# Optimization experiments

Measured on AMD Instinct MI355X. Metric: run time of the kernel, lower is better.

## Reference

```python
import jax, jax.numpy as jnp
import numpy as np


def setup_inputs() -> dict:
    key = jax.random.key(0)
    k1, k2, k3 = jax.random.split(key, 3)
    B, C, H, W = 64, 3, 512, 512
    n_segments, box, embed_dim = 1024, 16, 768
    img = jax.random.normal(k1, (B, C, H, W), dtype=jnp.float32)
    segments = jax.random.randint(k2, (B, H, W), 0, n_segments, dtype=jnp.int32)
    conv_w = jax.random.normal(k3, (embed_dim, C, box, box), dtype=jnp.float32) * 0.02
    return {"img": img, "segments": segments, "conv_w": conv_w, "n_segments": n_segments}


def reference(img, segments, conv_w, n_segments):
    # img: [B,C,H,W], segments: [B,H,W] int in [0,n_segments), conv_w: [E,C,box,box]
    B, C, H, W = img.shape
    E, _, box, _ = conv_w.shape
    half = box // 2

    # --- centroid per segment via scatter-add (equivalent to the one-hot mask-weighted sums) ---
    x_coords = jnp.broadcast_to(jnp.arange(W, dtype=jnp.float32)[None, :], (H, W)).reshape(-1)
    y_coords = jnp.broadcast_to(jnp.arange(H, dtype=jnp.float32)[:, None], (H, W)).reshape(-1)
    data = jnp.stack([x_coords, y_coords, jnp.ones_like(x_coords)], axis=-1)  # [H*W, 3]
    data = jnp.broadcast_to(data[None], (B, H * W, 3)).reshape(-1, 3)
    seg_ids = (segments.reshape(B, H * W) + jnp.arange(B, dtype=segments.dtype)[:, None] * n_segments).reshape(-1)
    sums = jax.ops.segment_sum(data, seg_ids, num_segments=B * n_segments)  # [B*S, 3]
    sums = sums.reshape(B, n_segments, 3)
    counts = jnp.clip(sums[..., 2], 1e-6, None)
    x_c = sums[..., 0] / counts  # [B, S]
    y_c = sums[..., 1] / counts

    # --- patch extraction at centroids from zero-padded image ---
    # x_min = floor((x_c + half) - half) = floor(x_c); x_c >= 0 so trunc == floor.
    x_min = jnp.floor(x_c).astype(jnp.int32)
    y_min = jnp.floor(y_c).astype(jnp.int32)
    img_padded = jnp.pad(img, ((0, 0), (0, 0), (half, half), (half, half)))

    def crop(im, y0, x0):  # im: [C, H+box, W+box]
        return jax.lax.dynamic_slice(im, (0, y0, x0), (C, box, box))

    crop_segs = jax.vmap(crop, in_axes=(None, 0, 0))          # over segments
    patches = jax.vmap(crop_segs)(img_padded, y_min, x_min)   # [B, S, C, box, box]

    # --- conv with kernel_size == box on box-sized patches == single dot per patch ---
    embeddings = jnp.einsum('bschw,echw->bse', patches, conv_w)  # [B, S, E]
    return embeddings
```

## Files before the change

kernel.cpp:

```cpp
#include <hip/hip_runtime.h>
#include <hip/hip_bf16.h>
#include <stdint.h>

#define B_   64
#define H_   512
#define W_   512
#define S_N  1024
#define E_N  768
#define K_N  768
#define HALF 8

typedef short bf16x8 __attribute__((ext_vector_type(8)));
typedef float f32x4  __attribute__((ext_vector_type(4)));
typedef float f32x4u __attribute__((ext_vector_type(4), aligned(4)));

__device__ __forceinline__ unsigned short f2bf(float f) {
  union { float f; unsigned u; } v; v.f = f;
  unsigned u = v.u;
  u += 0x7FFF + ((u >> 16) & 1);
  return (unsigned short)(u >> 16);
}

__global__ void k_accum_convw(const int* __restrict__ seg,
                              unsigned long long* __restrict__ partials,
                              const float* __restrict__ w,
                              unsigned short* __restrict__ wb) {
  __shared__ unsigned long long ls[S_N];
  const int bid = blockIdx.x;
  const int tid = threadIdx.x;
  if (bid >= 1024) {
    int idx = (bid - 1024) * 256 + tid;
    float4 v = ((const float4*)w)[idx];
    ushort4 o;
    o.x = f2bf(v.x); o.y = f2bf(v.y); o.z = f2bf(v.z); o.w = f2bf(v.w);
    ((ushort4*)wb)[idx] = o;
    return;
  }
  const int xblk = bid & 15;
  const int b    = bid >> 4;
  for (int i = tid; i < S_N; i += 256) ls[i] = 0ULL;
  __syncthreads();
  const int pix0 = xblk * 16384;
  const int4* segb = (const int4*)(seg + (size_t)b * (H_ * W_) + pix0);
  for (int it = 0; it < 16; ++it) {
    int4 s4 = segb[it * 256 + tid];
    int p0 = pix0 + (it * 256 + tid) * 4;
    unsigned long long base = ((unsigned long long)(unsigned)(p0 >> 9) << 39)
                            | ((unsigned long long)(unsigned)(p0 & (W_ - 1)) << 15)
                            | 1ULL;
    #pragma unroll
    for (int j = 0; j < 4; ++j) {
      int s = (&s4.x)[j];
      s = ((unsigned)s < S_N) ? s : 0;
      atomicAdd(&ls[s], base + ((unsigned long long)j << 15));
    }
  }
  __syncthreads();
  unsigned long long* gp = partials + ((size_t)b * 16 + xblk) * S_N;
  for (int s = tid; s < S_N; s += 256) gp[s] = ls[s];
}

__global__ __launch_bounds__(512) void k_gemmfg(
    const float* __restrict__ img,
    const unsigned long long* __restrict__ partials,
    const unsigned short* __restrict__ Bmat,
    float* __restrict__ out) {
  __shared__ unsigned short As[256 * 64];
  __shared__ unsigned short Bs[256 * 64];
  __shared__ int2 pc[256];
  const int tid  = threadIdx.x;
  const int wave = tid >> 6;
  const int lane = tid & 63;

  const int virt = (blockIdx.x & 7) * 96 + (blockIdx.x >> 3);
  const int bm = virt / 3;
  const int bn = virt - bm * 3;
  const int gm0 = bm * 256;
  const int gn0 = bn * 256;
  const int b   = bm >> 2;
  const float* ib = img + (size_t)b * 3 * H_ * W_;

  if (tid < 256) {
    const int s = (gm0 + tid) & (S_N - 1);
    unsigned c = 0, sx = 0, sy = 0;
    #pragma unroll
    for (int x = 0; x < 16; ++x) {
      unsigned long long v = partials[((size_t)b * 16 + x) * S_N + s];
      c  += (unsigned)(v & 0x7FFFULL);
      sx += (unsigned)((v >> 15) & 0xFFFFFFULL);
      sy += (unsigned)(v >> 39);
    }
    int xmin = 0, ymin = 0;
    if (c > 0) {
      float cf = (float)c;
      xmin = (int)floorf((float)sx / cf);
      ymin = (int)floorf((float)sy / cf);
    }
    pc[tid] = make_int2(xmin - HALF, ymin - HALF);
  }

  const int wr = wave >> 2;
  const int wc = wave & 3;
  const int rlo  = lane & 15;
  const int rsel = lane & 7;
  const int sub  = lane >> 4;
  int swz[2];
  swz[0] = ((0 + sub) ^ rsel) * 8;
  swz[1] = ((4 + sub) ^ rsel) * 8;

  f32x4 acc[8][4];
  #pragma unroll
  for (int i = 0; i < 8; ++i)
    #pragma unroll
    for (int j = 0; j < 4; ++j)
      acc[i][j] = (f32x4){0.f, 0.f, 0.f, 0.f};

  __syncthreads();

  for (int kt = 0; kt < 12; ++kt) {
    const int k0 = kt * 64;

    #pragma unroll
    for (int i = 0; i < 4; ++i) {
      int seg = i * 512 + tid;
      int row = seg >> 3;
      int csrc = (seg & 7) ^ (row & 7);
      const unsigned short* g = Bmat + (size_t)(gn0 + row) * K_N + k0 + csrc * 8;
      __builtin_amdgcn_global_load_lds((const __attribute__((address_space(1))) void*)g,
        (__attribute__((address_space(3))) void*)&Bs[(i * 512 + wave * 64) * 8], 16, 0, 0);
    }

    f32x4 ga[4][2];
    #pragma unroll
    for (int i = 0; i < 4; ++i) {
      int seg = i * 512 + tid;
      int row = seg >> 3;
      int cc  = seg & 7;
      int k = k0 + cc * 8;
      int ch = k >> 8, h = (k >> 4) & 15, w0 = k & 15;
      int2 p = pc[row];
      int y  = p.y + h;
      int x0 = p.x + w0;
      if (p.x >= 0 && p.x <= W_ - 16 && p.y >= 0 && p.y <= H_ - 16) {
        const float* rp = ib + (size_t)((ch << 9) + y) * W_ + x0;
        ga[i][0] = *(const f32x4u*)rp;
        ga[i][1] = *(const f32x4u*)(rp + 4);
      } else {
        bool yok = (unsigned)y < H_;
        const float* rp = ib + (size_t)((ch << 9) + (yok ? y : 0)) * W_;
        f32x4 lo, hi;
        #pragma unroll
        for (int j = 0; j < 4; ++j) {
          int x = x0 + j;
          lo[j] = (yok && (unsigned)x < W_) ? rp[x] : 0.f;
        }
        #pragma unroll
        for (int j = 0; j < 4; ++j) {
          int x = x0 + 4 + j;
          hi[j] = (yok && (unsigned)x < W_) ? rp[x] : 0.f;
        }
        ga[i][0] = lo;
        ga[i][1] = hi;
      }
    }
    #pragma unroll
    for (int i = 0; i < 4; ++i) {
      int seg = i * 512 + tid;
      int row = seg >> 3;
      int cc  = seg & 7;
      bf16x8 t;
      t[0] = (short)f2bf(ga[i][0][0]); t[1] = (short)f2bf(ga[i][0][1]);
      t[2] = (short)f2bf(ga[i][0][2]); t[3] = (short)f2bf(ga[i][0][3]);
      t[4] = (short)f2bf(ga[i][1][0]); t[5] = (short)f2bf(ga[i][1][1]);
      t[6] = (short)f2bf(ga[i][1][2]); t[7] = (short)f2bf(ga[i][1][3]);
      *(bf16x8*)&As[row * 64 + ((cc ^ (row & 7)) << 3)] = t;
    }

    asm volatile("s_waitcnt vmcnt(0) lgkmcnt(0)" ::: "memory");
    __syncthreads();

    #pragma unroll
    for (int kk = 0; kk < 2; ++kk) {
      bf16x8 av[8], bv[4];
      #pragma unroll
      for (int mi = 0; mi < 8; ++mi)
        av[mi] = *(const bf16x8*)&As[(wr * 128 + mi * 16 + rlo) * 64 + swz[kk]];
      #pragma unroll
      for (int ni = 0; ni < 4; ++ni)
        bv[ni] = *(const bf16x8*)&Bs[(wc * 64 + ni * 16 + rlo) * 64 + swz[kk]];
      __builtin_amdgcn_s_setprio(1);
      #pragma unroll
      for (int mi = 0; mi < 8; ++mi)
        #pragma unroll
        for (int ni = 0; ni < 4; ++ni)
          acc[mi][ni] = __builtin_amdgcn_mfma_f32_16x16x32_bf16(
              av[mi], bv[ni], acc[mi][ni], 0, 0, 0);
      __builtin_amdgcn_s_setprio(0);
    }

    __syncthreads();
  }

  const int row0 = gm0 + wr * 128 + (lane >> 4) * 4;
  const int col0 = gn0 + wc * 64 + (lane & 15);
  #pragma unroll
  for (int mi = 0; mi < 8; ++mi)
    #pragma unroll
    for (int ni = 0; ni < 4; ++ni)
      #pragma unroll
      for (int r = 0; r < 4; ++r)
        out[(size_t)(row0 + mi * 16 + r) * E_N + (col0 + ni * 16)] = acc[mi][ni][r];
}

extern "C" void kernel_launch(void* const* d_in, const int* in_sizes, int n_in,
                              void* d_out, int out_size, void* d_ws, size_t ws_size,
                              hipStream_t stream) {
  const float* img = (const float*)d_in[0];
  const int*   seg = (const int*)d_in[1];
  const float* cw  = (const float*)d_in[2];
  float* out = (float*)d_out;
  char* ws = (char*)d_ws;

  unsigned long long* partials = (unsigned long long*)ws;
  unsigned short* Bmat = (unsigned short*)(ws + 8388608);

  k_accum_convw<<<1600, 256, 0, stream>>>(seg, partials, cw, Bmat);
  k_gemmfg<<<768, 512, 0, stream>>>(img, partials, Bmat, out);
}
```

Before: 162.3 us.

## Prefetch next K-tile into registers while MFMA computes current tile

Restructures the GEMM main loop into a register-prefetch pipeline. The global loads for the next K-tile (image patch gather and B matrix) are issued before the MFMA work on the current tile, then converted and written to LDS after it. B loads switch from global_load_lds direct-to-LDS to register loads followed by LDS stores. Per-row pointers and in-bounds flags are hoisted out of the loop. The aim is to hide global memory latency behind compute, at the cost of more registers (which may limit occupancy at 512 threads) and an extra barrier per iteration.

```diff
diff --git a/kernel.cpp b/kernel.cpp
--- a/kernel.cpp
+++ b/kernel.cpp
@@ -60,7 +60,7 @@
   for (int s = tid; s < S_N; s += 256) gp[s] = ls[s];
 }
 
-__global__ __launch_bounds__(512) void k_gemmfg(
+__global__ __launch_bounds__(512) void k_gemmfg2(
     const float* __restrict__ img,
     const unsigned long long* __restrict__ partials,
     const unsigned short* __restrict__ Bmat,
@@ -117,67 +117,75 @@
 
   __syncthreads();
 
-  for (int kt = 0; kt < 12; ++kt) {
-    const int k0 = kt * 64;
-
+  const int cc0 = tid & 7;
+  const int rsub = tid >> 3;
+  int2 pi[4]; bool inti[4];
+  const float* arow[4];
+  const unsigned short* brow[4];
+  #pragma unroll
+  for (int i = 0; i < 4; ++i) {
+    int row = i * 64 + rsub;
+    int2 p = pc[row];
+    pi[i] = p;
+    inti[i] = (p.x >= 0 && p.x <= W_ - 16 && p.y >= 0 && p.y <= H_ - 16);
+    arow[i] = ib + (size_t)(inti[i] ? p.y : 0) * W_ + (inti[i] ? p.x : 0);
+    brow[i] = Bmat + (size_t)(gn0 + row) * K_N + (cc0 ^ (row & 7)) * 8;
+  }
+
+  f32x4 ga[4][2];
+  bf16x8 gb[4];
+
+  auto issue = [&](int k0) {
+    const int k = k0 + cc0 * 8;
+    const int ch = k >> 8, h = (k >> 4) & 15, w0 = k & 15;
+    const int roff = ((ch << 9) + h) * W_ + w0;
     #pragma unroll
     for (int i = 0; i < 4; ++i) {
-      int seg = i * 512 + tid;
-      int row = seg >> 3;
-      int csrc = (seg & 7) ^ (row & 7);
-      const unsigned short* g = Bmat + (size_t)(gn0 + row) * K_N + k0 + csrc * 8;
-      __builtin_amdgcn_global_load_lds((const __attribute__((address_space(1))) void*)g,
-        (__attribute__((address_space(3))) void*)&Bs[(i * 512 + wave * 64) * 8], 16, 0, 0);
-    }
-
-    f32x4 ga[4][2];
-    #pragma unroll
-    for (int i = 0; i < 4; ++i) {
-      int seg = i * 512 + tid;
-      int row = seg >> 3;
-      int cc  = seg & 7;
-      int k = k0 + cc * 8;
-      int ch = k >> 8, h = (k >> 4) & 15, w0 = k & 15;
-      int2 p = pc[row];
-      int y  = p.y + h;
-      int x0 = p.x + w0;
-      if (p.x >= 0 && p.x <= W_ - 16 && p.y >= 0 && p.y <= H_ - 16) {
-        const float* rp = ib + (size_t)((ch << 9) + y) * W_ + x0;
+      if (inti[i]) {
+        const float* rp = arow[i] + roff;
         ga[i][0] = *(const f32x4u*)rp;
         ga[i][1] = *(const f32x4u*)(rp + 4);
       } else {
+        int y = pi[i].y + h;
+        int x0 = pi[i].x + w0;
         bool yok = (unsigned)y < H_;
         const float* rp = ib + (size_t)((ch << 9) + (yok ? y : 0)) * W_;
-        f32x4 lo, hi;
         #pragma unroll
         for (int j = 0; j < 4; ++j) {
           int x = x0 + j;
-          lo[j] = (yok && (unsigned)x < W_) ? rp[x] : 0.f;
+          ga[i][0][j] = (yok && (unsigned)x < W_) ? rp[x] : 0.f;
         }
         #pragma unroll
         for (int j = 0; j < 4; ++j) {
           int x = x0 + 4 + j;
-          hi[j] = (yok && (unsigned)x < W_) ? rp[x] : 0.f;
+          ga[i][1][j] = (yok && (unsigned)x < W_) ? rp[x] : 0.f;
         }
-        ga[i][0] = lo;
-        ga[i][1] = hi;
       }
-    }
+      gb[i] = *(const bf16x8*)(brow[i] + k0);
+    }
+  };
+
+  auto writeTile = [&]() {
     #pragma unroll
     for (int i = 0; i < 4; ++i) {
-      int seg = i * 512 + tid;
-      int row = seg >> 3;
-      int cc  = seg & 7;
+      int row = i * 64 + rsub;
       bf16x8 t;
       t[0] = (short)f2bf(ga[i][0][0]); t[1] = (short)f2bf(ga[i][0][1]);
       t[2] = (short)f2bf(ga[i][0][2]); t[3] = (short)f2bf(ga[i][0][3]);
       t[4] = (short)f2bf(ga[i][1][0]); t[5] = (short)f2bf(ga[i][1][1]);
       t[6] = (short)f2bf(ga[i][1][2]); t[7] = (short)f2bf(ga[i][1][3]);
-      *(bf16x8*)&As[row * 64 + ((cc ^ (row & 7)) << 3)] = t;
-    }
-
-    asm volatile("s_waitcnt vmcnt(0) lgkmcnt(0)" ::: "memory");
-    __syncthreads();
+      *(bf16x8*)&As[row * 64 + ((cc0 ^ (row & 7)) << 3)] = t;
+      *(bf16x8*)&Bs[(i * 512 + tid) * 8] = gb[i];
+    }
+  };
+
+  issue(0);
+  writeTile();
+  __syncthreads();
+
+  for (int kt = 0; kt < 12; ++kt) {
+    if (kt + 1 < 12) issue((kt + 1) * 64);
+    __builtin_amdgcn_sched_barrier(0);
 
     #pragma unroll
     for (int kk = 0; kk < 2; ++kk) {
@@ -198,7 +206,11 @@
       __builtin_amdgcn_s_setprio(0);
     }
 
-    __syncthreads();
+    if (kt + 1 < 12) {
+      __syncthreads();
+      writeTile();
+      __syncthreads();
+    }
   }
 
   const int row0 = gm0 + wr * 128 + (lane >> 4) * 4;
@@ -225,5 +237,5 @@
   unsigned short* Bmat = (unsigned short*)(ws + 8388608);
 
   k_accum_convw<<<1600, 256, 0, stream>>>(seg, partials, cw, Bmat);
-  k_gemmfg<<<768, 512, 0, stream>>>(img, partials, Bmat, out);
-}
+  k_gemmfg2<<<768, 512, 0, stream>>>(img, partials, Bmat, out);
+}
```

New measurement: 181.1 us. +11.5%, slower.

## Shrink GEMM tile to 128x128 with 256 threads and hoist patch row pointers

Applied to the files above, without the earlier changes.

The fused gather-GEMM moves from 256x256 tiles with 512 threads to 128x128 tiles with 256 threads, launched as 3072 blocks, with launch bounds asking for 3 blocks per CU. Per-row patch origin, in-bounds flag and base pointer are now computed once before the K loop instead of every iteration. The goal is more resident blocks and better latency hiding on the scattered image gathers, plus less address arithmetic per iteration. In exchange, each output tile does less reuse, so the image patches are gathered six times per row block instead of three, and Bmat is read more often.

```diff
diff --git a/kernel.cpp b/kernel.cpp
--- a/kernel.cpp
+++ b/kernel.cpp
@@ -60,27 +60,27 @@
   for (int s = tid; s < S_N; s += 256) gp[s] = ls[s];
 }
 
-__global__ __launch_bounds__(512) void k_gemmfg(
+__global__ __launch_bounds__(256, 3) void k_gemmfg4(
     const float* __restrict__ img,
     const unsigned long long* __restrict__ partials,
     const unsigned short* __restrict__ Bmat,
     float* __restrict__ out) {
-  __shared__ unsigned short As[256 * 64];
-  __shared__ unsigned short Bs[256 * 64];
-  __shared__ int2 pc[256];
+  __shared__ unsigned short As[128 * 64];
+  __shared__ unsigned short Bs[128 * 64];
+  __shared__ int2 pc[128];
   const int tid  = threadIdx.x;
   const int wave = tid >> 6;
   const int lane = tid & 63;
 
-  const int virt = (blockIdx.x & 7) * 96 + (blockIdx.x >> 3);
-  const int bm = virt / 3;
-  const int bn = virt - bm * 3;
-  const int gm0 = bm * 256;
-  const int gn0 = bn * 256;
-  const int b   = bm >> 2;
+  const int virt = (blockIdx.x & 7) * 384 + (blockIdx.x >> 3);
+  const int bm = virt / 6;
+  const int bn = virt - bm * 6;
+  const int gm0 = bm * 128;
+  const int gn0 = bn * 128;
+  const int b   = bm >> 3;
   const float* ib = img + (size_t)b * 3 * H_ * W_;
 
-  if (tid < 256) {
+  if (tid < 128) {
     const int s = (gm0 + tid) & (S_N - 1);
     unsigned c = 0, sx = 0, sy = 0;
     #pragma unroll
@@ -99,8 +99,8 @@
     pc[tid] = make_int2(xmin - HALF, ymin - HALF);
   }
 
-  const int wr = wave >> 2;
-  const int wc = wave & 3;
+  const int wr = wave >> 1;
+  const int wc = wave & 1;
   const int rlo  = lane & 15;
   const int rsel = lane & 7;
   const int sub  = lane >> 4;
@@ -108,72 +108,77 @@
   swz[0] = ((0 + sub) ^ rsel) * 8;
   swz[1] = ((4 + sub) ^ rsel) * 8;
 
-  f32x4 acc[8][4];
+  f32x4 acc[4][4];
   #pragma unroll
-  for (int i = 0; i < 8; ++i)
+  for (int i = 0; i < 4; ++i)
     #pragma unroll
     for (int j = 0; j < 4; ++j)
       acc[i][j] = (f32x4){0.f, 0.f, 0.f, 0.f};
 
   __syncthreads();
 
+  const int c0 = tid & 7;
+  const int rr = tid >> 3;
+  int2 pi[4]; bool inti[4];
+  const float* arow[4];
+  #pragma unroll
+  for (int i = 0; i < 4; ++i) {
+    int row = i * 32 + rr;
+    int2 p = pc[row];
+    pi[i] = p;
+    inti[i] = (p.x >= 0 && p.x <= W_ - 16 && p.y >= 0 && p.y <= H_ - 16);
+    arow[i] = ib + (size_t)(inti[i] ? p.y : 0) * W_ + (inti[i] ? p.x : 0);
+  }
+
   for (int kt = 0; kt < 12; ++kt) {
     const int k0 = kt * 64;
 
     #pragma unroll
     for (int i = 0; i < 4; ++i) {
-      int seg = i * 512 + tid;
+      int seg = i * 256 + tid;
       int row = seg >> 3;
       int csrc = (seg & 7) ^ (row & 7);
       const unsigned short* g = Bmat + (size_t)(gn0 + row) * K_N + k0 + csrc * 8;
       __builtin_amdgcn_global_load_lds((const __attribute__((address_space(1))) void*)g,
-        (__attribute__((address_space(3))) void*)&Bs[(i * 512 + wave * 64) * 8], 16, 0, 0);
-    }
-
-    f32x4 ga[4][2];
-    #pragma unroll
-    for (int i = 0; i < 4; ++i) {
-      int seg = i * 512 + tid;
-      int row = seg >> 3;
-      int cc  = seg & 7;
-      int k = k0 + cc * 8;
-      int ch = k >> 8, h = (k >> 4) & 15, w0 = k & 15;
-      int2 p = pc[row];
-      int y  = p.y + h;
-      int x0 = p.x + w0;
-      if (p.x >= 0 && p.x <= W_ - 16 && p.y >= 0 && p.y <= H_ - 16) {
-        const float* rp = ib + (size_t)((ch << 9) + y) * W_ + x0;
-        ga[i][0] = *(const f32x4u*)rp;
-        ga[i][1] = *(const f32x4u*)(rp + 4);
-      } else {
-        bool yok = (unsigned)y < H_;
-        const float* rp = ib + (size_t)((ch << 9) + (yok ? y : 0)) * W_;
+        (__attribute__((address_space(3))) void*)&Bs[(i * 256 + wave * 64) * 8], 16, 0, 0);
+    }
+
+    {
+      const int k  = k0 + c0 * 8;
+      const int ch = k >> 8, hh = (k >> 4) & 15, w0 = k & 15;
+      const int roff = ((ch << 9) + hh) * W_ + w0;
+      #pragma unroll
+      for (int i = 0; i < 4; ++i) {
+        int row = i * 32 + rr;
         f32x4 lo, hi;
+        if (inti[i]) {
+          const float* rp = arow[i] + roff;
+          lo = *(const f32x4u*)rp;
+          hi = *(const f32x4u*)(rp + 4);
+        } else {
+          int y = pi[i].y + hh;
+          int x0 = pi[i].x + w0;
+          bool yok = (unsigned)y < H_;
+          const float* rp = ib + (size_t)((ch << 9) + (yok ? y : 0)) * W_;
+          #pragma unroll
+          for (int j = 0; j < 4; ++j) {
+            int x = x0 + j;
+            lo[j] = (yok && (unsigned)x < W_) ? rp[x] : 0.f;
+          }
+          #pragma unroll
+          for (int j = 0; j < 4; ++j) {
+            int x = x0 + 4 + j;
+            hi[j] = (yok && (unsigned)x < W_) ? rp[x] : 0.f;
+          }
+        }
+        bf16x8 t;
         #pragma unroll
         for (int j = 0; j < 4; ++j) {
-          int x = x0 + j;
-          lo[j] = (yok && (unsigned)x < W_) ? rp[x] : 0.f;
+          t[j]     = (short)f2bf(lo[j]);
+          t[4 + j] = (short)f2bf(hi[j]);
         }
-        #pragma unroll
-        for (int j = 0; j < 4; ++j) {
-          int x = x0 + 4 + j;
-          hi[j] = (yok && (unsigned)x < W_) ? rp[x] : 0.f;
-        }
-        ga[i][0] = lo;
-        ga[i][1] = hi;
+        *(bf16x8*)&As[row * 64 + ((c0 ^ (row & 7)) << 3)] = t;
       }
-    }
-    #pragma unroll
-    for (int i = 0; i < 4; ++i) {
-      int seg = i * 512 + tid;
-      int row = seg >> 3;
-      int cc  = seg & 7;
-      bf16x8 t;
-      t[0] = (short)f2bf(ga[i][0][0]); t[1] = (short)f2bf(ga[i][0][1]);
-      t[2] = (short)f2bf(ga[i][0][2]); t[3] = (short)f2bf(ga[i][0][3]);
-      t[4] = (short)f2bf(ga[i][1][0]); t[5] = (short)f2bf(ga[i][1][1]);
-      t[6] = (short)f2bf(ga[i][1][2]); t[7] = (short)f2bf(ga[i][1][3]);
-      *(bf16x8*)&As[row * 64 + ((cc ^ (row & 7)) << 3)] = t;
     }
 
     asm volatile("s_waitcnt vmcnt(0) lgkmcnt(0)" ::: "memory");
@@ -181,16 +186,16 @@
 
     #pragma unroll
     for (int kk = 0; kk < 2; ++kk) {
-      bf16x8 av[8], bv[4];
-      #pragma unroll
-      for (int mi = 0; mi < 8; ++mi)
-        av[mi] = *(const bf16x8*)&As[(wr * 128 + mi * 16 + rlo) * 64 + swz[kk]];
+      bf16x8 av[4], bv[4];
+      #pragma unroll
+      for (int mi = 0; mi < 4; ++mi)
+        av[mi] = *(const bf16x8*)&As[(wr * 64 + mi * 16 + rlo) * 64 + swz[kk]];
       #pragma unroll
       for (int ni = 0; ni < 4; ++ni)
         bv[ni] = *(const bf16x8*)&Bs[(wc * 64 + ni * 16 + rlo) * 64 + swz[kk]];
       __builtin_amdgcn_s_setprio(1);
       #pragma unroll
-      for (int mi = 0; mi < 8; ++mi)
+      for (int mi = 0; mi < 4; ++mi)
         #pragma unroll
         for (int ni = 0; ni < 4; ++ni)
           acc[mi][ni] = __builtin_amdgcn_mfma_f32_16x16x32_bf16(
@@ -201,10 +206,10 @@
     __syncthreads();
   }
 
-  const int row0 = gm0 + wr * 128 + (lane >> 4) * 4;
+  const int row0 = gm0 + wr * 64 + (lane >> 4) * 4;
   const int col0 = gn0 + wc * 64 + (lane & 15);
   #pragma unroll
-  for (int mi = 0; mi < 8; ++mi)
+  for (int mi = 0; mi < 4; ++mi)
     #pragma unroll
     for (int ni = 0; ni < 4; ++ni)
       #pragma unroll
@@ -225,5 +230,5 @@
   unsigned short* Bmat = (unsigned short*)(ws + 8388608);
 
   k_accum_convw<<<1600, 256, 0, stream>>>(seg, partials, cw, Bmat);
-  k_gemmfg<<<768, 512, 0, stream>>>(img, partials, Bmat, out);
-}
+  k_gemmfg4<<<3072, 256, 0, stream>>>(img, partials, Bmat, out);
+}
```

Measured after the change: 179.9 us. 10.8% more time.
